# Performance work log

Hardware: AMD Instinct MI355X
Metric: run time of the kernel (lower is better)

The kernel has to match this reference:

```python
import jax, jax.numpy as jnp
import numpy as np

B, S, D, H = 2, 2048, 1024, 16
DH = D // H


def setup_inputs() -> dict:
    key = jax.random.key(0)
    ks = jax.random.split(key, 7)
    scale = 1.0 / np.sqrt(D)
    queries = jax.random.normal(ks[0], (B, S, D), dtype=jnp.float32)
    keys_ = jax.random.normal(ks[1], (B, S, D), dtype=jnp.float32)
    values = jax.random.normal(ks[2], (B, S, D), dtype=jnp.float32)
    mask = jnp.tril(jnp.ones((S, S), dtype=jnp.int32))[None, None]  # causal [1,1,S,S]
    Wq = jax.random.normal(ks[3], (D, D), dtype=jnp.float32) * scale
    Wk = jax.random.normal(ks[4], (D, D), dtype=jnp.float32) * scale
    Wv = jax.random.normal(ks[5], (D, D), dtype=jnp.float32) * scale
    Wo = jax.random.normal(ks[6], (D, D), dtype=jnp.float32) * scale
    return {"queries": queries, "keys": keys_, "values": values, "mask": mask,
            "Wq": Wq, "Wk": Wk, "Wv": Wv, "Wo": Wo}


def reference(queries, keys, values, mask, Wq, Wk, Wv, Wo):
    # linear projections (nn.Linear, no bias): x @ W.T
    def split_heads(x, W):
        return (x @ W.T).reshape(B, -1, H, DH).transpose(0, 2, 1, 3)  # [B,H,S,DH]

    q = split_heads(queries, Wq)
    k = split_heads(keys, Wk)
    v = split_heads(values, Wv)

    scores = jnp.einsum('bhqd,bhkd->bhqk', q, k) / jnp.sqrt(jnp.float32(DH))
    scores = jnp.where(mask == 0, jnp.float32(-jnp.inf), scores)
    weights = jax.nn.softmax(scores, axis=-1)  # dropout p=0.0 -> identity
    out = jnp.einsum('bhqk,bhkd->bhqd', weights, v)
    out = out.transpose(0, 2, 1, 3).reshape(B, -1, D)
    return out @ Wo.T
```

## Files before the change

### kernel.cpp

```cpp
#include <hip/hip_runtime.h>
#include <hip/hip_bf16.h>


typedef unsigned short u16;
typedef __attribute__((ext_vector_type(8))) short bf16x8;
typedef __attribute__((ext_vector_type(4))) float f32x4;
typedef __attribute__((ext_vector_type(4))) short s16x4;

#define DEVI static __device__ __forceinline__
#define SCL 0.18033688011112042f
#define LDSW 40
#define GLDS(g, l) __builtin_amdgcn_global_load_lds( \
    (const __attribute__((address_space(1))) unsigned*)(g), \
    (__attribute__((address_space(3))) unsigned*)(l), 16, 0, 0)

DEVI u16 f2bf(float f) {
  __hip_bfloat16 h = __float2bfloat16(f);
  union { __hip_bfloat16 h; u16 u; } c; c.h = h;
  return c.u;
}

DEVI bf16x8 cvt8(f32x4 a, f32x4 b) {
  bf16x8 r;
  r[0] = (short)f2bf(a[0]); r[1] = (short)f2bf(a[1]);
  r[2] = (short)f2bf(a[2]); r[3] = (short)f2bf(a[3]);
  r[4] = (short)f2bf(b[0]); r[5] = (short)f2bf(b[1]);
  r[6] = (short)f2bf(b[2]); r[7] = (short)f2bf(b[3]);
  return r;
}

template <int F32>
DEVI bf16x8 lda8(const void* base, size_t off) {
  if constexpr (!F32) {
    return *(const bf16x8*)((const u16*)base + off);
  } else {
    const float* p = (const float*)base + off;
    return cvt8(*(const f32x4*)p, *(const f32x4*)(p + 4));
  }
}

template <int F32>
DEVI void load_pair(f32x4* lo, f32x4* hi, bf16x8* bb, const void* P,
                    size_t o0, size_t o1) {
  if constexpr (F32) {
    const float* p0 = (const float*)P + o0;
    const float* p1 = (const float*)P + o1;
    lo[0] = *(const f32x4*)p0; hi[0] = *(const f32x4*)(p0 + 4);
    lo[1] = *(const f32x4*)p1; hi[1] = *(const f32x4*)(p1 + 4);
  } else {
    bb[0] = *(const bf16x8*)((const u16*)P + o0);
    bb[1] = *(const bf16x8*)((const u16*)P + o1);
  }
}

template <int F32>
DEVI void finish_pair(f32x4* lo, f32x4* hi, bf16x8* bb, u16* dst, int le0, int le1) {
  if constexpr (F32) { bb[0] = cvt8(lo[0], hi[0]); bb[1] = cvt8(lo[1], hi[1]); }
  *(bf16x8*)(dst + le0) = bb[0];
  *(bf16x8*)(dst + le1) = bb[1];
}

DEVI void vwait4() { asm volatile("s_waitcnt vmcnt(4)" ::: "memory"); }
DEVI void vwait2() { asm volatile("s_waitcnt vmcnt(2)" ::: "memory"); }
DEVI void vwait0() { asm volatile("s_waitcnt vmcnt(0)" ::: "memory"); }
DEVI void bar_lds() {
  asm volatile("s_waitcnt lgkmcnt(0)" ::: "memory");
  asm volatile("s_barrier" ::: "memory");
}

template <int MODE, int O32>
DEVI void epilogue(f32x4 (&acc)[4][4], void* C, int tileM, int tileN,
                   int wr, int wc, int lr, int lg, float oscale) {
  constexpr int N = 1024;
  if constexpr (MODE == 0) {
#pragma unroll
    for (int m = 0; m < 4; ++m) {
      const int row0 = tileM + wr + m * 16 + lg * 4;
#pragma unroll
      for (int n = 0; n < 4; ++n) {
        const int col = tileN + wc + n * 16 + lr;
#pragma unroll
        for (int j = 0; j < 4; ++j) {
          if constexpr (O32)
            ((float*)C)[(size_t)(row0 + j) * N + col] = acc[m][n][j] * oscale;
          else
            ((u16*)C)[(size_t)(row0 + j) * N + col] = f2bf(acc[m][n][j] * oscale);
        }
      }
    }
  } else if constexpr (MODE == 1) {
    u16* Cv = (u16*)C;
#pragma unroll
    for (int m = 0; m < 4; ++m) {
      const int row0 = tileM + wr + m * 16 + lg * 4;
      const int bb = row0 >> 11, s0 = row0 & 2047;
#pragma unroll
      for (int n = 0; n < 4; ++n) {
        const int col = tileN + wc + n * 16 + lr;
        s16x4 pk;
#pragma unroll
        for (int j = 0; j < 4; ++j) pk[j] = (short)f2bf(acc[m][n][j]);
        *(s16x4*)(Cv + ((size_t)(col + (bb << 10)) << 11) + s0) = pk;
      }
    }
  } else {
    u16* Cv = (u16*)C;
#pragma unroll
    for (int m = 0; m < 4; ++m) {
      const int row0 = tileM + wr + m * 16 + lg * 4;
      const int bb = row0 >> 11, s0 = row0 & 2047;
#pragma unroll
      for (int n = 0; n < 4; ++n) {
        const int col = tileN + wc + n * 16 + lr;
        const size_t base = ((size_t)((bb << 4) + (col >> 6)) * 2048 + s0) * 64 + (col & 63);
#pragma unroll
        for (int j = 0; j < 4; ++j)
          Cv[base + (size_t)j * 64] = f2bf(acc[m][n][j]);
      }
    }
  }
}

template <int F32>
__global__ void __launch_bounds__(256)
cvt_w3(const void* w0, const void* w1, const void* w2,
       u16* o0, u16* o1, u16* o2) {
  const int y = blockIdx.y;
  const void* w = (y == 0) ? w0 : ((y == 1) ? w1 : w2);
  u16* o = (y == 0) ? o0 : ((y == 1) ? o1 : o2);
  const int r = blockIdx.x * 256 + threadIdx.x;
  const int p = r >> 14, t = (r >> 9) & 31, row = (r >> 2) & 127, g = r & 3;
  const int col = t * 32 + ((g ^ ((row >> 1) & 3)) << 3);
  const size_t src = ((size_t)(p * 128 + row) << 10) + col;
  *(bf16x8*)(o + (size_t)r * 8) = lda8<F32>(w, src);
}

template <int A32, int MODE, int O32>
DEVI void gemm_core(u16* sA0, u16* sA1, u16* sW0, u16* sW1,
                    const void* A, const u16* Wb, void* C,
                    int tileM, int tileN, float oscale) {
  constexpr int K = 1024;
  const int tid = threadIdx.x;
  const int lane = tid & 63;
  const int wave = tid >> 6;
  const int wr = (wave >> 1) * 64;
  const int wc = (wave & 1) * 64;
  const int lr = lane & 15, lg = lane >> 4;

  f32x4 acc[4][4] = {};

  const int e0 = tid * 8;
  const int e1 = 2048 + tid * 8;
  const int r0 = e0 >> 5, c0 = e0 & 31;
  const int r1 = e1 >> 5, c1 = e1 & 31;
  const int le0 = r0 * LDSW + c0;
  const int le1 = r1 * LDSW + c1;
  const size_t oA0 = (size_t)(tileM + r0) * K + c0;
  const size_t oA1 = (size_t)(tileM + r1) * K + c1;

  const u16* WB = Wb + ((size_t)(tileN >> 7) * 32) * 4096 + tid * 8;
  u16* dW0 = sW0 + wave * 512;
  u16* dW1 = sW1 + wave * 512;
#define STAGE_W(tt, dst) { GLDS(WB + (size_t)(tt) * 4096, dst); \
                           GLDS(WB + (size_t)(tt) * 4096 + 2048, (dst) + 2048); }

  f32x4 eLo[2], eHi[2], oLo[2], oHi[2];
  bf16x8 eB[2], oB[2];

  load_pair<A32>(eLo, eHi, eB, A, oA0, oA1);
  STAGE_W(0, dW0);
  finish_pair<A32>(eLo, eHi, eB, sA0, le0, le1);
  load_pair<A32>(oLo, oHi, oB, A, oA0 + 32, oA1 + 32);
  if constexpr (A32) vwait4(); else vwait2();
  bar_lds();

#pragma unroll 1
  for (int it = 0; it < 16; ++it) {
    {
      const int tE = it * 2;
      STAGE_W(tE + 1, dW1);
      bf16x8 af[4], bfr[4];
#pragma unroll
      for (int m = 0; m < 4; ++m)
        af[m] = *(const bf16x8*)(sA0 + (wr + m * 16 + lr) * LDSW + lg * 8);
#pragma unroll
      for (int n = 0; n < 4; ++n) {
        const int row = wc + n * 16 + lr;
        bfr[n] = *(const bf16x8*)(sW0 + row * 32 + ((lg ^ ((row >> 1) & 3)) << 3));
      }
      if (it < 15) load_pair<A32>(eLo, eHi, eB, A, oA0 + (tE + 2) * 32, oA1 + (tE + 2) * 32);
#pragma unroll
      for (int m = 0; m < 4; ++m)
#pragma unroll
        for (int n = 0; n < 4; ++n)
          acc[m][n] = __builtin_amdgcn_mfma_f32_16x16x32_bf16(af[m], bfr[n], acc[m][n], 0, 0, 0);
      finish_pair<A32>(oLo, oHi, oB, sA1, le0, le1);
      if (it < 15) { if constexpr (A32) vwait4(); else vwait2(); } else vwait0();
      bar_lds();
    }
    {
      const int tO = it * 2 + 1;
      if (it < 15) STAGE_W(tO + 1, dW0);
      bf16x8 af[4], bfr[4];
#pragma unroll
      for (int m = 0; m < 4; ++m)
        af[m] = *(const bf16x8*)(sA1 + (wr + m * 16 + lr) * LDSW + lg * 8);
#pragma unroll
      for (int n = 0; n < 4; ++n) {
        const int row = wc + n * 16 + lr;
        bfr[n] = *(const bf16x8*)(sW1 + row * 32 + ((lg ^ ((row >> 1) & 3)) << 3));
      }
      if (it < 15) load_pair<A32>(oLo, oHi, oB, A, oA0 + (tO + 2) * 32, oA1 + (tO + 2) * 32);
#pragma unroll
      for (int m = 0; m < 4; ++m)
#pragma unroll
        for (int n = 0; n < 4; ++n)
          acc[m][n] = __builtin_amdgcn_mfma_f32_16x16x32_bf16(af[m], bfr[n], acc[m][n], 0, 0, 0);
      if (it < 15) {
        finish_pair<A32>(eLo, eHi, eB, sA0, le0, le1);
        if constexpr (A32) vwait4(); else vwait2();
      } else {
        vwait0();
      }
      bar_lds();
    }
  }
#undef STAGE_W
  epilogue<MODE, O32>(acc, C, tileM, tileN, wr, wc, lr, lg, oscale);
}

DEVI void tile_remap(int& tileM, int& tileN) {
  const int i = blockIdx.x + 8 * blockIdx.y;
  const int c = i & 7, s = i >> 3;
  tileM = (c * 4 + (s & 3)) * 128;
  tileN = (s >> 2) * 128;
}

template <int IN32>
__global__ void __launch_bounds__(256, 3)
gemm_qkv(const void* __restrict__ q, const u16* __restrict__ WqB, u16* __restrict__ Qp,
         const void* __restrict__ k, const u16* __restrict__ WkB, u16* __restrict__ Kh,
         const void* __restrict__ v, const u16* __restrict__ WvB, u16* __restrict__ Vt) {
  __shared__ __align__(16) u16 sA[2][128 * LDSW];
  __shared__ __align__(16) u16 sW[2][128 * 32];
  int tileM, tileN;
  tile_remap(tileM, tileN);
  if (blockIdx.z == 0)
    gemm_core<IN32, 0, 0>(sA[0], sA[1], sW[0], sW[1], q, WqB, Qp, tileM, tileN, SCL);
  else if (blockIdx.z == 1)
    gemm_core<IN32, 2, 0>(sA[0], sA[1], sW[0], sW[1], k, WkB, Kh, tileM, tileN, 1.f);
  else
    gemm_core<IN32, 1, 0>(sA[0], sA[1], sW[0], sW[1], v, WvB, Vt, tileM, tileN, 1.f);
}

template <int O32>
__global__ void __launch_bounds__(256, 3)
gemm_out(const u16* __restrict__ A, const u16* __restrict__ WoB, void* __restrict__ C) {
  __shared__ __align__(16) u16 sA[2][128 * LDSW];
  __shared__ __align__(16) u16 sW[2][128 * 32];
  int tileM, tileN;
  tile_remap(tileM, tileN);
  gemm_core<0, 0, O32>(sA[0], sA[1], sW[0], sW[1], A, WoB, C, tileM, tileN, 1.f);
}

DEVI void stage_klds4(const u16* __restrict__ Kb, const u16* __restrict__ Vb,
                      u16* sKb, u16* sVb, int kt, int w, int lane) {
  const int kr = w * 8 + (lane >> 3);
  const int kg = (lane & 7) ^ (lane >> 3);
  const u16* gk = Kb + (size_t)(kt + kr) * 64 + kg * 8;
  const int vr = w * 16 + (lane >> 2);
  const int vg = (lane & 3) ^ ((vr >> 1) & 3);
  const u16* gv = Vb + (size_t)vr * 2048 + kt + vg * 8;
  GLDS(gk, sKb + w * 512);
  GLDS(gv, sVb + w * 512);
}

__global__ void __launch_bounds__(256, 4)
attn_kernel(const u16* Qp, const u16* __restrict__ Kh,
            const u16* __restrict__ Vt, u16* AO) {
  __shared__ __align__(16) u16 sK[3][2048];
  __shared__ __align__(16) u16 sV[3][2048];
  const int tid = threadIdx.x;
  const int lane = tid & 63;
  const int w = tid >> 6;
  const int lr = lane & 15;
  const int lg = lane >> 4;

  const int id = blockIdx.x;
  const int xcd = id & 7;
  const int slot = id >> 3;
  const int bh = xcd * 4 + (slot & 3);
  const int bd = 31 - (slot >> 2);
  const int b = bh >> 4;
  const int h = bh & 15;
  const int r0 = bd * 64;

  const u16* Kb = Kh + (size_t)bh * 2048 * 64;
  const u16* Vb = Vt + (size_t)bh * 64 * 2048;

  const int qrow = r0 + w * 16 + lr;
  const u16* Qw = Qp + ((size_t)(b * 2048 + qrow) << 10) + h * 64;
  const bf16x8 qf0 = *(const bf16x8*)(Qw + lg * 8);
  const bf16x8 qf1 = *(const bf16x8*)(Qw + 32 + lg * 8);

  f32x4 o[4] = {};
  float mr = -INFINITY, ls = 0.f;
  const int nt = 2 * bd + 2;

  stage_klds4(Kb, Vb, sK[0], sV[0], 0, w, lane);

#pragma unroll 1
  for (int t = 0; t < nt; ++t) {
    if (t + 1 < nt) {
      const int bi = (t + 1) % 3;
      stage_klds4(Kb, Vb, sK[bi], sV[bi], (t + 1) * 32, w, lane);
      vwait2();
    } else {
      vwait0();
    }
    asm volatile("s_barrier" ::: "memory");
    __builtin_amdgcn_s_setprio(1);

    {
      const int bi = t % 3;
      const u16* sKb = sK[bi];
      const u16* sVb = sV[bi];
      const int sw = lr & 7;
      const bf16x8 kf0 = *(const bf16x8*)(sKb + lr * 64 + ((lg ^ sw) * 8));
      const bf16x8 kf1 = *(const bf16x8*)(sKb + lr * 64 + (((4 + lg) ^ sw) * 8));
      const bf16x8 kf2 = *(const bf16x8*)(sKb + (16 + lr) * 64 + ((lg ^ sw) * 8));
      const bf16x8 kf3 = *(const bf16x8*)(sKb + (16 + lr) * 64 + (((4 + lg) ^ sw) * 8));

      const f32x4 z = {};
      f32x4 s0 = __builtin_amdgcn_mfma_f32_16x16x32_bf16(kf0, qf0, z, 0, 0, 0);
      s0 = __builtin_amdgcn_mfma_f32_16x16x32_bf16(kf1, qf1, s0, 0, 0, 0);
      f32x4 s1 = __builtin_amdgcn_mfma_f32_16x16x32_bf16(kf2, qf0, z, 0, 0, 0);
      s1 = __builtin_amdgcn_mfma_f32_16x16x32_bf16(kf3, qf1, s1, 0, 0, 0);

      float p[8];
#pragma unroll
      for (int j = 0; j < 4; ++j) { p[j] = s0[j]; p[4 + j] = s1[j]; }
      if (t >= nt - 2) {
        const int kt0 = t * 32;
#pragma unroll
        for (int j = 0; j < 4; ++j) {
          if (kt0 + lg * 4 + j > qrow)      p[j] = -INFINITY;
          if (kt0 + 16 + lg * 4 + j > qrow) p[4 + j] = -INFINITY;
        }
      }

      const float tm = fmaxf(fmaxf(fmaxf(p[0], p[1]), fmaxf(p[2], p[3])),
                             fmaxf(fmaxf(p[4], p[5]), fmaxf(p[6], p[7])));
      if (!__all(tm <= mr + 11.5f)) {
        float tr_ = fmaxf(tm, __shfl_xor(tm, 16));
        tr_ = fmaxf(tr_, __shfl_xor(tr_, 32));
        const float mn = fmaxf(mr, tr_);
        const float fac = exp2f(mr - mn);
        mr = mn;
        ls *= fac;
#pragma unroll
        for (int j = 0; j < 4; ++j) {
          const float fj = __shfl(fac, lg * 4 + j);
#pragma unroll
          for (int d = 0; d < 4; ++d) o[d][j] *= fj;
        }
      }

#pragma unroll
      for (int i = 0; i < 8; ++i) p[i] = exp2f(p[i] - mr);
      ls += ((p[0] + p[1]) + (p[2] + p[3])) + ((p[4] + p[5]) + (p[6] + p[7]));

      bf16x8 pa;
#pragma unroll
      for (int i = 0; i < 8; ++i) pa[i] = (short)f2bf(p[i]);

      const int s2 = (lr >> 1) & 3;
#pragma unroll
      for (int d = 0; d < 4; ++d) {
        const u16* vrow = sVb + (16 * d + lr) * 32;
        const s16x4 v0 = *(const s16x4*)(vrow + (((lg >> 1) ^ s2) * 8) + (lg & 1) * 4);
        const s16x4 v1 = *(const s16x4*)(vrow + ((((lg >> 1) + 2) ^ s2) * 8) + (lg & 1) * 4);
        bf16x8 vf;
        vf[0] = v0[0]; vf[1] = v0[1]; vf[2] = v0[2]; vf[3] = v0[3];
        vf[4] = v1[0]; vf[5] = v1[1]; vf[6] = v1[2]; vf[7] = v1[3];
        o[d] = __builtin_amdgcn_mfma_f32_16x16x32_bf16(pa, vf, o[d], 0, 0, 0);
      }
    }
    __builtin_amdgcn_s_setprio(0);
  }

  float lt = ls + __shfl_xor(ls, 16);
  lt += __shfl_xor(lt, 32);
  const size_t orow = (size_t)(b * 2048 + r0 + w * 16 + lg * 4);
#pragma unroll
  for (int j = 0; j < 4; ++j) {
    const float inv = 1.0f / __shfl(lt, lg * 4 + j);
#pragma unroll
    for (int d = 0; d < 4; ++d)
      AO[(orow + j) * 1024 + h * 64 + 16 * d + lr] = f2bf(o[d][j] * inv);
  }
}

static int bytes_per_elem(void* p, long long n, void* pnext) {
  if (pnext) {
    ptrdiff_t d = (char*)pnext - (char*)p;
    if (d == n * 2) return 2;
    if (d == n * 4) return 4;
  }
  size_t sz = 0;
  if (hipMemPtrGetInfo(p, &sz) == hipSuccess && sz >= (size_t)(n * 2)) {
    if (sz < (size_t)(n * 4)) return 2;
    if (sz <= (size_t)(n * 8)) return 4;
  }
  return 4;
}

extern "C" void kernel_launch(void* const* d_in, const int* in_sizes, int n_in,
                              void* d_out, int out_size, void* d_ws, size_t ws_size,
                              hipStream_t stream) {
  void* q  = d_in[0];
  void* k  = d_in[1];
  void* v  = d_in[2];
  void* wq = d_in[4];
  void* wk = d_in[5];
  void* wv = d_in[6];
  void* wo = d_in[7];

  const int in32 = bytes_per_elem(q, in_sizes[0], k) == 4;
  const int w32  = bytes_per_elem(wq, in_sizes[4], wk) == 4;
  const int o32  = bytes_per_elem(d_out, out_size, nullptr) == 4;

  const size_t SZ = (size_t)4096 * 1024;
  const size_t WZ = (size_t)1024 * 1024;
  u16* Qp = (u16*)d_ws;
  u16* Kh = Qp + SZ;
  u16* Vt = (u16*)d_out;
  u16* AO = Qp;
  u16* WqB = Vt + SZ;
  u16* WkB = WqB + WZ;
  u16* WvB = WkB + WZ;
  u16* WoB = Kh;

  if (w32) cvt_w3<1><<<dim3(512, 3), 256, 0, stream>>>(wq, wk, wv, WqB, WkB, WvB);
  else     cvt_w3<0><<<dim3(512, 3), 256, 0, stream>>>(wq, wk, wv, WqB, WkB, WvB);

  if (in32)
    gemm_qkv<1><<<dim3(8, 32, 3), 256, 0, stream>>>(q, WqB, Qp, k, WkB, Kh, v, WvB, Vt);
  else
    gemm_qkv<0><<<dim3(8, 32, 3), 256, 0, stream>>>(q, WqB, Qp, k, WkB, Kh, v, WvB, Vt);

  attn_kernel<<<dim3(1024), 256, 0, stream>>>(Qp, Kh, Vt, AO);

  if (w32) cvt_w3<1><<<dim3(512, 1), 256, 0, stream>>>(wo, wo, wo, WoB, WoB, WoB);
  else     cvt_w3<0><<<dim3(512, 1), 256, 0, stream>>>(wo, wo, wo, WoB, WoB, WoB);

  if (o32) gemm_out<1><<<dim3(8, 32), 256, 0, stream>>>(AO, WoB, d_out);
  else     gemm_out<0><<<dim3(8, 32), 256, 0, stream>>>(AO, WoB, d_out);
}
```

Before: 116.7 us.

## Load weight fragments directly from global into registers, dropping LDS staging

```diff
diff --git a/kernel.cpp b/kernel.cpp
--- a/kernel.cpp
+++ b/kernel.cpp
@@ -60,7 +60,6 @@
   *(bf16x8*)(dst + le1) = bb[1];
 }
 
-DEVI void vwait4() { asm volatile("s_waitcnt vmcnt(4)" ::: "memory"); }
 DEVI void vwait2() { asm volatile("s_waitcnt vmcnt(2)" ::: "memory"); }
 DEVI void vwait0() { asm volatile("s_waitcnt vmcnt(0)" ::: "memory"); }
 DEVI void bar_lds() {
@@ -130,13 +129,13 @@
   u16* o = (y == 0) ? o0 : ((y == 1) ? o1 : o2);
   const int r = blockIdx.x * 256 + threadIdx.x;
   const int p = r >> 14, t = (r >> 9) & 31, row = (r >> 2) & 127, g = r & 3;
-  const int col = t * 32 + ((g ^ ((row >> 1) & 3)) << 3);
+  const int col = t * 32 + g * 8;
   const size_t src = ((size_t)(p * 128 + row) << 10) + col;
   *(bf16x8*)(o + (size_t)r * 8) = lda8<F32>(w, src);
 }
 
 template <int A32, int MODE, int O32>
-DEVI void gemm_core(u16* sA0, u16* sA1, u16* sW0, u16* sW1,
+DEVI void gemm_core(u16* sA0, u16* sA1,
                     const void* A, const u16* Wb, void* C,
                     int tileM, int tileN, float oscale) {
   constexpr int K = 1024;
@@ -158,74 +157,57 @@
   const size_t oA0 = (size_t)(tileM + r0) * K + c0;
   const size_t oA1 = (size_t)(tileM + r1) * K + c1;
 
-  const u16* WB = Wb + ((size_t)(tileN >> 7) * 32) * 4096 + tid * 8;
-  u16* dW0 = sW0 + wave * 512;
-  u16* dW1 = sW1 + wave * 512;
-#define STAGE_W(tt, dst) { GLDS(WB + (size_t)(tt) * 4096, dst); \
-                           GLDS(WB + (size_t)(tt) * 4096 + 2048, (dst) + 2048); }
+  const u16* WL = Wb + (size_t)(tileN >> 7) * 131072 + (size_t)(wc + lr) * 32 + lg * 8;
+#define LOADW(dst, tt) { \
+    _Pragma("unroll") \
+    for (int n = 0; n < 4; ++n) \
+      dst[n] = *(const bf16x8*)(WL + (size_t)(tt) * 4096 + n * 512); }
 
   f32x4 eLo[2], eHi[2], oLo[2], oHi[2];
   bf16x8 eB[2], oB[2];
+  bf16x8 wf[4];
 
   load_pair<A32>(eLo, eHi, eB, A, oA0, oA1);
-  STAGE_W(0, dW0);
   finish_pair<A32>(eLo, eHi, eB, sA0, le0, le1);
   load_pair<A32>(oLo, oHi, oB, A, oA0 + 32, oA1 + 32);
-  if constexpr (A32) vwait4(); else vwait2();
   bar_lds();
 
 #pragma unroll 1
   for (int it = 0; it < 16; ++it) {
     {
       const int tE = it * 2;
-      STAGE_W(tE + 1, dW1);
-      bf16x8 af[4], bfr[4];
+      LOADW(wf, tE);
+      bf16x8 af[4];
 #pragma unroll
       for (int m = 0; m < 4; ++m)
         af[m] = *(const bf16x8*)(sA0 + (wr + m * 16 + lr) * LDSW + lg * 8);
-#pragma unroll
-      for (int n = 0; n < 4; ++n) {
-        const int row = wc + n * 16 + lr;
-        bfr[n] = *(const bf16x8*)(sW0 + row * 32 + ((lg ^ ((row >> 1) & 3)) << 3));
-      }
       if (it < 15) load_pair<A32>(eLo, eHi, eB, A, oA0 + (tE + 2) * 32, oA1 + (tE + 2) * 32);
 #pragma unroll
       for (int m = 0; m < 4; ++m)
 #pragma unroll
         for (int n = 0; n < 4; ++n)
-          acc[m][n] = __builtin_amdgcn_mfma_f32_16x16x32_bf16(af[m], bfr[n], acc[m][n], 0, 0, 0);
+          acc[m][n] = __builtin_amdgcn_mfma_f32_16x16x32_bf16(af[m], wf[n], acc[m][n], 0, 0, 0);
       finish_pair<A32>(oLo, oHi, oB, sA1, le0, le1);
-      if (it < 15) { if constexpr (A32) vwait4(); else vwait2(); } else vwait0();
       bar_lds();
     }
     {
       const int tO = it * 2 + 1;
-      if (it < 15) STAGE_W(tO + 1, dW0);
-      bf16x8 af[4], bfr[4];
+      LOADW(wf, tO);
+      bf16x8 af[4];
 #pragma unroll
       for (int m = 0; m < 4; ++m)
         af[m] = *(const bf16x8*)(sA1 + (wr + m * 16 + lr) * LDSW + lg * 8);
-#pragma unroll
-      for (int n = 0; n < 4; ++n) {
-        const int row = wc + n * 16 + lr;
-        bfr[n] = *(const bf16x8*)(sW1 + row * 32 + ((lg ^ ((row >> 1) & 3)) << 3));
-      }
       if (it < 15) load_pair<A32>(oLo, oHi, oB, A, oA0 + (tO + 2) * 32, oA1 + (tO + 2) * 32);
 #pragma unroll
       for (int m = 0; m < 4; ++m)
 #pragma unroll
         for (int n = 0; n < 4; ++n)
-          acc[m][n] = __builtin_amdgcn_mfma_f32_16x16x32_bf16(af[m], bfr[n], acc[m][n], 0, 0, 0);
-      if (it < 15) {
-        finish_pair<A32>(eLo, eHi, eB, sA0, le0, le1);
-        if constexpr (A32) vwait4(); else vwait2();
-      } else {
-        vwait0();
-      }
+          acc[m][n] = __builtin_amdgcn_mfma_f32_16x16x32_bf16(af[m], wf[n], acc[m][n], 0, 0, 0);
+      if (it < 15) finish_pair<A32>(eLo, eHi, eB, sA0, le0, le1);
       bar_lds();
     }
   }
-#undef STAGE_W
+#undef LOADW
   epilogue<MODE, O32>(acc, C, tileM, tileN, wr, wc, lr, lg, oscale);
 }
 
@@ -242,25 +224,23 @@
          const void* __restrict__ k, const u16* __restrict__ WkB, u16* __restrict__ Kh,
          const void* __restrict__ v, const u16* __restrict__ WvB, u16* __restrict__ Vt) {
   __shared__ __align__(16) u16 sA[2][128 * LDSW];
-  __shared__ __align__(16) u16 sW[2][128 * 32];
   int tileM, tileN;
   tile_remap(tileM, tileN);
   if (blockIdx.z == 0)
-    gemm_core<IN32, 0, 0>(sA[0], sA[1], sW[0], sW[1], q, WqB, Qp, tileM, tileN, SCL);
+    gemm_core<IN32, 0, 0>(sA[0], sA[1], q, WqB, Qp, tileM, tileN, SCL);
   else if (blockIdx.z == 1)
-    gemm_core<IN32, 2, 0>(sA[0], sA[1], sW[0], sW[1], k, WkB, Kh, tileM, tileN, 1.f);
+    gemm_core<IN32, 2, 0>(sA[0], sA[1], k, WkB, Kh, tileM, tileN, 1.f);
   else
-    gemm_core<IN32, 1, 0>(sA[0], sA[1], sW[0], sW[1], v, WvB, Vt, tileM, tileN, 1.f);
+    gemm_core<IN32, 1, 0>(sA[0], sA[1], v, WvB, Vt, tileM, tileN, 1.f);
 }
 
 template <int O32>
 __global__ void __launch_bounds__(256, 3)
 gemm_out(const u16* __restrict__ A, const u16* __restrict__ WoB, void* __restrict__ C) {
   __shared__ __align__(16) u16 sA[2][128 * LDSW];
-  __shared__ __align__(16) u16 sW[2][128 * 32];
   int tileM, tileN;
   tile_remap(tileM, tileN);
-  gemm_core<0, 0, O32>(sA[0], sA[1], sW[0], sW[1], A, WoB, C, tileM, tileN, 1.f);
+  gemm_core<0, 0, O32>(sA[0], sA[1], A, WoB, C, tileM, tileN, 1.f);
 }
 
 DEVI void stage_klds4(const u16* __restrict__ Kb, const u16* __restrict__ Vb,
```

Result: slower. 126.1 us (+8.0%).
